# Kernel tuning notes

Measured on AMD Instinct MI355X. Metric: run time of the kernel, lower is better.

Reference implementation:

```python
import jax, jax.numpy as jnp
import numpy as np

N_BONDS = 16777216
N_ATOMS = 1048576
N_TYPES = 16


def setup_inputs() -> dict:
    key = jax.random.key(0)
    k1, k2, k3, k4, k5, k6 = jax.random.split(key, 6)
    # bond orders kept strictly positive so BO**p_be2 and its grad are finite
    bo_sigma = jax.random.uniform(k1, (N_BONDS,), jnp.float32, 0.05, 1.0)
    bo_pi = jax.random.uniform(k2, (N_BONDS,), jnp.float32, 0.05, 1.0)
    bo_pipi = jax.random.uniform(k3, (N_BONDS,), jnp.float32, 0.05, 1.0)
    bond_type = jax.random.randint(k4, (N_BONDS,), 0, N_TYPES, jnp.int32)
    atom_i = jax.random.randint(k5, (N_BONDS,), 0, N_ATOMS, jnp.int32)
    # columns: De_sigma, De_pi, De_pipi, p_be1, p_be2 (positive, O(1))
    bond_params = jax.random.uniform(k6, (N_TYPES, 5), jnp.float32, 0.1, 1.0)
    return {
        "bond_type": bond_type,
        "atom_i": atom_i,
        "bo_sigma": bo_sigma,
        "bo_pi": bo_pi,
        "bo_pipi": bo_pipi,
        "bond_params": bond_params,
        "n_atoms": N_ATOMS,
    }


def reference(bond_type, atom_i, bo_sigma, bo_pi, bo_pipi, bond_params, n_atoms):
    # Gather per-bond-type parameters: [E, 5]
    p = bond_params[bond_type]
    de_s, de_p, de_pp, p_be1, p_be2 = (p[:, 0], p[:, 1], p[:, 2], p[:, 3], p[:, 4])
    # ReaxFF bond energy per bond
    e_bond = (-de_s * bo_sigma * jnp.exp(p_be1 * (1.0 - bo_sigma ** p_be2))
              - de_p * bo_pi
              - de_pp * bo_pipi)
    # Scatter-reduce to per-atom energy
    e_atom = jax.ops.segment_sum(e_bond, atom_i, num_segments=n_atoms)
    return e_atom
```

## Files before the change

kernel.cpp:

```cpp
#include <hip/hip_runtime.h>


typedef float f32x4 __attribute__((ext_vector_type(4)));
typedef int   i32x4 __attribute__((ext_vector_type(4)));
typedef unsigned u32;

#define NB     512
#define RANGE  2048
#define SHIFT  11
#define CB     8192
#define TB     256
#define PADQ   8u

__device__ __forceinline__ u32 f32_to_bf16_bits(float f) {
    u32 u = __float_as_uint(f);
    return ((u + 0x7FFFu + ((u >> 16) & 1u)) >> 16) & 0xFFFFu;
}

__global__ __launch_bounds__(TB) void count_kernel(
        const i32x4* __restrict__ atom_i, u32* __restrict__ counts,
        int round_start) {
    __shared__ u32 hist[4][NB];
    int tid = threadIdx.x, w = tid >> 6;
    for (int i = tid; i < 4 * NB; i += TB) ((u32*)hist)[i] = 0u;
    __syncthreads();
    long base4 = ((long)round_start + (long)blockIdx.x * CB) >> 2;
#pragma unroll
    for (int it = 0; it < CB / (TB * 4); ++it) {
        i32x4 a = __builtin_nontemporal_load(&atom_i[base4 + it * TB + tid]);
        atomicAdd(&hist[w][(u32)a.x >> SHIFT], 1u);
        atomicAdd(&hist[w][(u32)a.y >> SHIFT], 1u);
        atomicAdd(&hist[w][(u32)a.z >> SHIFT], 1u);
        atomicAdd(&hist[w][(u32)a.w >> SHIFT], 1u);
    }
    __syncthreads();
    for (int b = tid; b < NB; b += TB)
        counts[(size_t)blockIdx.x * NB + b] =
            hist[0][b] + hist[1][b] + hist[2][b] + hist[3][b];
}

__global__ __launch_bounds__(TB) void scan_cols_kernel(
        const u32* __restrict__ counts, u32* __restrict__ offs,
        u32* __restrict__ total, int nsb) {
    __shared__ u32 sc[TB];
    int b = blockIdx.x, t = threadIdx.x;
    int vpt = nsb >> 8;
    u32 v[16];
    u32 s = 0;
    for (int k = 0; k < vpt; ++k) {
        u32 c = counts[(size_t)(t * vpt + k) * NB + b];
        c = (c + PADQ - 1u) & ~(PADQ - 1u);
        v[k] = s; s += c;
    }
    sc[t] = s;
    __syncthreads();
    for (int off = 1; off < TB; off <<= 1) {
        u32 u = (t >= off) ? sc[t - off] : 0u;
        __syncthreads();
        sc[t] += u;
        __syncthreads();
    }
    u32 excl = sc[t] - s;
    for (int k = 0; k < vpt; ++k)
        offs[(size_t)(t * vpt + k) * NB + b] = excl + v[k];
    if (t == TB - 1) total[b] = sc[t];
}

__global__ __launch_bounds__(TB, 4) void partition_kernel(
        const i32x4* __restrict__ bt, const i32x4* __restrict__ ai,
        const f32x4* __restrict__ bs_, const f32x4* __restrict__ bp_,
        const f32x4* __restrict__ bpp_, const float* __restrict__ bond_params,
        const u32* __restrict__ counts, const u32* __restrict__ offs,
        const u32* __restrict__ total, u32* __restrict__ arena,
        int round_start) {
    __shared__ u32   sorted[CB];
    __shared__ u32   cnt[NB], cur[NB], gstart[NB];
    __shared__ u32   scanb[TB];
    __shared__ float4 sp_a[16];
    __shared__ float  sp_b[16];

    int tid = threadIdx.x, sb = blockIdx.x;
    if (tid < 16) {
        const float* p = bond_params + tid * 5;
        sp_a[tid] = make_float4(p[0], p[1], p[2], p[3]);
        sp_b[tid] = p[4];
    }
    u32 c0 = counts[(size_t)sb * NB + 2 * tid];
    u32 c1 = counts[(size_t)sb * NB + 2 * tid + 1];
    cnt[2 * tid] = c0; cnt[2 * tid + 1] = c1;
    scanb[tid] = c0 + c1;
    __syncthreads();
    for (int off = 1; off < TB; off <<= 1) {
        u32 u = (tid >= off) ? scanb[tid - off] : 0u;
        __syncthreads();
        scanb[tid] += u;
        __syncthreads();
    }
    u32 excl = scanb[tid] - (c0 + c1);
    cur[2 * tid] = excl; cur[2 * tid + 1] = excl + c0;
    __syncthreads();
    u32 t0 = total[2 * tid], t1 = total[2 * tid + 1];
    scanb[tid] = t0 + t1;
    __syncthreads();
    for (int off = 1; off < TB; off <<= 1) {
        u32 u = (tid >= off) ? scanb[tid - off] : 0u;
        __syncthreads();
        scanb[tid] += u;
        __syncthreads();
    }
    u32 excl2 = scanb[tid] - (t0 + t1);
    gstart[2 * tid]     = excl2 + offs[(size_t)sb * NB + 2 * tid];
    gstart[2 * tid + 1] = excl2 + t0 + offs[(size_t)sb * NB + 2 * tid + 1];
    __syncthreads();

    long base4 = ((long)round_start + (long)sb * CB) >> 2;
#pragma unroll
    for (int it = 0; it < CB / (TB * 4); ++it) {
        long idx = base4 + it * TB + tid;
        i32x4 t  = __builtin_nontemporal_load(&bt[idx]);
        i32x4 a  = __builtin_nontemporal_load(&ai[idx]);
        f32x4 s  = __builtin_nontemporal_load(&bs_[idx]);
        f32x4 p  = __builtin_nontemporal_load(&bp_[idx]);
        f32x4 pp = __builtin_nontemporal_load(&bpp_[idx]);
#pragma unroll
        for (int k = 0; k < 4; ++k) {
            u32 ak = (u32)a[k];
            float4 pa = sp_a[t[k]];
            float  pb = sp_b[t[k]];
            float pw = __powf(s[k], pb);
            float e  = -pa.x * s[k] * __expf(pa.w * (1.0f - pw))
                       - pa.y * p[k] - pa.z * pp[k];
            u32 b = ak >> SHIFT;
            u32 pos = atomicAdd(&cur[b], 1u);
            sorted[pos] = ((ak & (RANGE - 1u)) << 16) | f32_to_bf16_bits(e);
        }
    }
    __syncthreads();

    int w = tid >> 6, lane = tid & 63;
    int gi = lane >> 4, j0 = lane & 15;
    for (int b = w * 4 + gi; b < NB; b += 16) {
        u32 end = cur[b], len = cnt[b], ls = end - len;
        u32 plen = (len + PADQ - 1u) & ~(PADQ - 1u);
        u32 g = gstart[b];
        for (u32 j = j0; j < plen; j += 16u)
            arena[g + j] = (j < len) ? sorted[ls + j] : 0u;
    }
}

__global__ __launch_bounds__(TB, 4) void accum_kernel(
        const u32* __restrict__ arena, const u32* __restrict__ total,
        float* __restrict__ out, int add_prev) {
    __shared__ float acc[4][RANGE];
    __shared__ u32 red[TB];
    int tid = threadIdx.x, w = tid >> 6, b = blockIdx.x;
    u32 part = 0;
    for (int i = tid; i < b; i += TB) part += total[i];
    red[tid] = part;
    for (int i = tid; i < RANGE; i += TB) {
        acc[0][i] = 0.f; acc[1][i] = 0.f; acc[2][i] = 0.f; acc[3][i] = 0.f;
    }
    __syncthreads();
    for (int s = TB / 2; s > 0; s >>= 1) {
        if (tid < s) red[tid] += red[tid + s];
        __syncthreads();
    }
    u32 s0 = red[0];
    u32 n  = total[b];
    const uint4* src = (const uint4*)(arena + s0);
    for (u32 j = tid; j < (n >> 2); j += TB) {
        uint4 e = src[j];
        if (e.x) atomicAdd(&acc[w][e.x >> 16], __uint_as_float((e.x & 0xFFFFu) << 16));
        if (e.y) atomicAdd(&acc[w][e.y >> 16], __uint_as_float((e.y & 0xFFFFu) << 16));
        if (e.z) atomicAdd(&acc[w][e.z >> 16], __uint_as_float((e.z & 0xFFFFu) << 16));
        if (e.w) atomicAdd(&acc[w][e.w >> 16], __uint_as_float((e.w & 0xFFFFu) << 16));
    }
    __syncthreads();
    size_t ob = (size_t)b * RANGE;
    for (int i = tid; i < RANGE; i += TB) {
        float v = acc[0][i] + acc[1][i] + acc[2][i] + acc[3][i];
        if (add_prev) v += out[ob + i];
        out[ob + i] = v;
    }
}

__global__ __launch_bounds__(TB) void zero_kernel(f32x4* __restrict__ p, int n4) {
    int i = blockIdx.x * blockDim.x + threadIdx.x;
    if (i < n4) p[i] = (f32x4)(0.f);
}

__global__ __launch_bounds__(TB) void atomic_fallback_kernel(
        const i32x4* __restrict__ bt, const i32x4* __restrict__ ai,
        const f32x4* __restrict__ bs_, const f32x4* __restrict__ bp_,
        const f32x4* __restrict__ bpp_, const float* __restrict__ bond_params,
        float* __restrict__ out, int n4) {
    __shared__ float sp[80];
    if (threadIdx.x < 80) sp[threadIdx.x] = bond_params[threadIdx.x];
    __syncthreads();
    int i = blockIdx.x * blockDim.x + threadIdx.x;
    if (i >= n4) return;
    i32x4 t  = bt[i]; i32x4 a = ai[i];
    f32x4 s  = bs_[i]; f32x4 p = bp_[i]; f32x4 pp = bpp_[i];
#pragma unroll
    for (int k = 0; k < 4; ++k) {
        const float* pr = sp + t[k] * 5;
        float pw = __powf(s[k], pr[4]);
        float e  = -pr[0] * s[k] * __expf(pr[3] * (1.0f - pw))
                   - pr[1] * p[k] - pr[2] * pp[k];
        unsafeAtomicAdd(&out[a[k]], e);
    }
}

extern "C" void kernel_launch(void* const* d_in, const int* in_sizes, int n_in,
                              void* d_out, int out_size, void* d_ws, size_t ws_size,
                              hipStream_t stream) {
    const int*   bond_type   = (const int*)  d_in[0];
    const int*   atom_i      = (const int*)  d_in[1];
    const float* bo_sigma    = (const float*)d_in[2];
    const float* bo_pi       = (const float*)d_in[3];
    const float* bo_pipi     = (const float*)d_in[4];
    const float* bond_params = (const float*)d_in[5];
    float*       e_atom      = (float*)d_out;

    const int n_bonds = in_sizes[0];
    const int n_atoms = out_size;

    int NR = 0;
    if (n_atoms == (NB << SHIFT)) {
        const int cands[5] = {1, 2, 4, 8, 16};
        for (int ci = 0; ci < 5; ++ci) {
            int r = cands[ci];
            if (n_bonds % (r * CB)) continue;
            int cpr = n_bonds / r, nsb = cpr / CB;
            if (nsb % 256 || nsb < 256 || nsb > 4096) continue;
            size_t arena_worst = (size_t)cpr + (size_t)(PADQ - 1) * NB * nsb;
            size_t need = arena_worst * 4 + 2 * (size_t)nsb * NB * 4 + (size_t)NB * 4;
            if (need <= ws_size) { NR = r; break; }
        }
    }

    if (NR) {
        const int cpr = n_bonds / NR, nsb = cpr / CB;
        size_t arena_worst = (size_t)cpr + (size_t)(PADQ - 1) * NB * nsb;
        u32* arena  = (u32*)d_ws;
        u32* counts = arena + arena_worst;
        u32* offs   = counts + (size_t)nsb * NB;
        u32* total  = offs + (size_t)nsb * NB;
        for (int r = 0; r < NR; ++r) {
            int rs = r * cpr;
            count_kernel<<<nsb, TB, 0, stream>>>((const i32x4*)atom_i, counts, rs);
            scan_cols_kernel<<<NB, TB, 0, stream>>>(counts, offs, total, nsb);
            partition_kernel<<<nsb, TB, 0, stream>>>(
                (const i32x4*)bond_type, (const i32x4*)atom_i,
                (const f32x4*)bo_sigma, (const f32x4*)bo_pi, (const f32x4*)bo_pipi,
                bond_params, counts, offs, total, arena, rs);
            accum_kernel<<<NB, TB, 0, stream>>>(arena, total, e_atom, r ? 1 : 0);
        }
    } else {
        int zn4 = n_atoms / 4;
        zero_kernel<<<(zn4 + TB - 1) / TB, TB, 0, stream>>>((f32x4*)e_atom, zn4);
        int n4 = n_bonds / 4;
        atomic_fallback_kernel<<<(n4 + TB - 1) / TB, TB, 0, stream>>>(
            (const i32x4*)bond_type, (const i32x4*)atom_i,
            (const f32x4*)bo_sigma, (const f32x4*)bo_pi, (const f32x4*)bo_pipi,
            bond_params, e_atom, n4);
    }
}
```

Baseline: 439.3 us.

## Shrink partition chunk, hoist bucket base scan, use 16-bit counts and wave scans

Adds a 4096-bond chunk option for the count and partition kernels and prefers it, so each partition block uses half the LDS and more blocks fit per CU (launch bound raised to 7). The per-block scan of bucket totals moves into a separate single-block base_kernel that writes gbase, which accum also reads instead of re-reducing totals. Per-block counts are stored as u16 and the LDS Hillis-Steele scans become wave-shuffle scans. The cost is an extra tiny launch per round, twice as many chunks with more padded slots in the arena, and more count/offs traffic in the column scan.

New measurement: 457.5 us. +4.2%, slower.

```diff
diff --git a/kernel.cpp b/kernel.cpp
--- a/kernel.cpp
+++ b/kernel.cpp
@@ -4,11 +4,11 @@
 typedef float f32x4 __attribute__((ext_vector_type(4)));
 typedef int   i32x4 __attribute__((ext_vector_type(4)));
 typedef unsigned u32;
+typedef unsigned short u16;
 
 #define NB     512
 #define RANGE  2048
 #define SHIFT  11
-#define CB     8192
 #define TB     256
 #define PADQ   8u
 
@@ -17,16 +17,33 @@
     return ((u + 0x7FFFu + ((u >> 16) & 1u)) >> 16) & 0xFFFFu;
 }
 
+__device__ __forceinline__ u32 block_excl_scan(u32 v, u32* wsum, int tid) {
+    u32 s = v;
+#pragma unroll
+    for (int off = 1; off < 64; off <<= 1) {
+        u32 n = __shfl_up(s, off);
+        if ((tid & 63) >= off) s += n;
+    }
+    if ((tid & 63) == 63) wsum[tid >> 6] = s;
+    __syncthreads();
+    int w = tid >> 6;
+    u32 wb = 0;
+#pragma unroll
+    for (int ww = 0; ww < 3; ++ww) wb += (ww < w) ? wsum[ww] : 0u;
+    return wb + s - v;
+}
+
+template<int CBK>
 __global__ __launch_bounds__(TB) void count_kernel(
-        const i32x4* __restrict__ atom_i, u32* __restrict__ counts,
+        const i32x4* __restrict__ atom_i, u16* __restrict__ counts,
         int round_start) {
     __shared__ u32 hist[4][NB];
     int tid = threadIdx.x, w = tid >> 6;
     for (int i = tid; i < 4 * NB; i += TB) ((u32*)hist)[i] = 0u;
     __syncthreads();
-    long base4 = ((long)round_start + (long)blockIdx.x * CB) >> 2;
-#pragma unroll
-    for (int it = 0; it < CB / (TB * 4); ++it) {
+    long base4 = ((long)round_start + (long)blockIdx.x * CBK) >> 2;
+#pragma unroll
+    for (int it = 0; it < CBK / (TB * 4); ++it) {
         i32x4 a = __builtin_nontemporal_load(&atom_i[base4 + it * TB + tid]);
         atomicAdd(&hist[w][(u32)a.x >> SHIFT], 1u);
         atomicAdd(&hist[w][(u32)a.y >> SHIFT], 1u);
@@ -36,11 +53,11 @@
     __syncthreads();
     for (int b = tid; b < NB; b += TB)
         counts[(size_t)blockIdx.x * NB + b] =
-            hist[0][b] + hist[1][b] + hist[2][b] + hist[3][b];
+            (u16)(hist[0][b] + hist[1][b] + hist[2][b] + hist[3][b]);
 }
 
 __global__ __launch_bounds__(TB) void scan_cols_kernel(
-        const u32* __restrict__ counts, u32* __restrict__ offs,
+        const u16* __restrict__ counts, u32* __restrict__ offs,
         u32* __restrict__ total, int nsb) {
     __shared__ u32 sc[TB];
     int b = blockIdx.x, t = threadIdx.x;
@@ -66,16 +83,27 @@
     if (t == TB - 1) total[b] = sc[t];
 }
 
-__global__ __launch_bounds__(TB, 4) void partition_kernel(
+__global__ __launch_bounds__(TB) void base_kernel(
+        const u32* __restrict__ total, u32* __restrict__ gbase) {
+    __shared__ u32 wsum[4];
+    int t = threadIdx.x;
+    u32 t0 = total[2 * t], t1 = total[2 * t + 1];
+    u32 excl = block_excl_scan(t0 + t1, wsum, t);
+    gbase[2 * t]     = excl;
+    gbase[2 * t + 1] = excl + t0;
+}
+
+template<int CBK, int MINB>
+__global__ __launch_bounds__(TB, MINB) void partition_kernel(
         const i32x4* __restrict__ bt, const i32x4* __restrict__ ai,
         const f32x4* __restrict__ bs_, const f32x4* __restrict__ bp_,
         const f32x4* __restrict__ bpp_, const float* __restrict__ bond_params,
-        const u32* __restrict__ counts, const u32* __restrict__ offs,
-        const u32* __restrict__ total, u32* __restrict__ arena,
+        const u16* __restrict__ counts, const u32* __restrict__ offs,
+        const u32* __restrict__ gbase, u32* __restrict__ arena,
         int round_start) {
-    __shared__ u32   sorted[CB];
-    __shared__ u32   cnt[NB], cur[NB], gstart[NB];
-    __shared__ u32   scanb[TB];
+    __shared__ u32   sorted[CBK];
+    __shared__ u32   start_[NB], cur[NB];
+    __shared__ u32   wsum[4];
     __shared__ float4 sp_a[16];
     __shared__ float  sp_b[16];
 
@@ -85,37 +113,16 @@
         sp_a[tid] = make_float4(p[0], p[1], p[2], p[3]);
         sp_b[tid] = p[4];
     }
-    u32 c0 = counts[(size_t)sb * NB + 2 * tid];
-    u32 c1 = counts[(size_t)sb * NB + 2 * tid + 1];
-    cnt[2 * tid] = c0; cnt[2 * tid + 1] = c1;
-    scanb[tid] = c0 + c1;
-    __syncthreads();
-    for (int off = 1; off < TB; off <<= 1) {
-        u32 u = (tid >= off) ? scanb[tid - off] : 0u;
-        __syncthreads();
-        scanb[tid] += u;
-        __syncthreads();
-    }
-    u32 excl = scanb[tid] - (c0 + c1);
-    cur[2 * tid] = excl; cur[2 * tid + 1] = excl + c0;
-    __syncthreads();
-    u32 t0 = total[2 * tid], t1 = total[2 * tid + 1];
-    scanb[tid] = t0 + t1;
-    __syncthreads();
-    for (int off = 1; off < TB; off <<= 1) {
-        u32 u = (tid >= off) ? scanb[tid - off] : 0u;
-        __syncthreads();
-        scanb[tid] += u;
-        __syncthreads();
-    }
-    u32 excl2 = scanb[tid] - (t0 + t1);
-    gstart[2 * tid]     = excl2 + offs[(size_t)sb * NB + 2 * tid];
-    gstart[2 * tid + 1] = excl2 + t0 + offs[(size_t)sb * NB + 2 * tid + 1];
-    __syncthreads();
-
-    long base4 = ((long)round_start + (long)sb * CB) >> 2;
-#pragma unroll
-    for (int it = 0; it < CB / (TB * 4); ++it) {
+    u32 c01 = ((const u32*)(counts + (size_t)sb * NB))[tid];
+    u32 c0 = c01 & 0xFFFFu, c1 = c01 >> 16;
+    u32 excl = block_excl_scan(c0 + c1, wsum, tid);
+    start_[2 * tid]     = excl;       cur[2 * tid]     = excl;
+    start_[2 * tid + 1] = excl + c0;  cur[2 * tid + 1] = excl + c0;
+    __syncthreads();
+
+    long base4 = ((long)round_start + (long)sb * CBK) >> 2;
+#pragma unroll
+    for (int it = 0; it < CBK / (TB * 4); ++it) {
         long idx = base4 + it * TB + tid;
         i32x4 t  = __builtin_nontemporal_load(&bt[idx]);
         i32x4 a  = __builtin_nontemporal_load(&ai[idx]);
@@ -137,35 +144,29 @@
     }
     __syncthreads();
 
+    constexpr int LG  = (CBK >= 8192) ? 16 : 8;
+    constexpr int GPW = 64 / LG;
     int w = tid >> 6, lane = tid & 63;
-    int gi = lane >> 4, j0 = lane & 15;
-    for (int b = w * 4 + gi; b < NB; b += 16) {
-        u32 end = cur[b], len = cnt[b], ls = end - len;
+    int gi = lane / LG, j0 = lane % LG;
+    for (int b = w * GPW + gi; b < NB; b += 4 * GPW) {
+        u32 end = cur[b], ls = start_[b], len = end - ls;
         u32 plen = (len + PADQ - 1u) & ~(PADQ - 1u);
-        u32 g = gstart[b];
-        for (u32 j = j0; j < plen; j += 16u)
+        u32 g = gbase[b] + offs[(size_t)sb * NB + b];
+        for (u32 j = j0; j < plen; j += LG)
             arena[g + j] = (j < len) ? sorted[ls + j] : 0u;
     }
 }
 
 __global__ __launch_bounds__(TB, 4) void accum_kernel(
         const u32* __restrict__ arena, const u32* __restrict__ total,
-        float* __restrict__ out, int add_prev) {
+        const u32* __restrict__ gbase, float* __restrict__ out, int add_prev) {
     __shared__ float acc[4][RANGE];
-    __shared__ u32 red[TB];
     int tid = threadIdx.x, w = tid >> 6, b = blockIdx.x;
-    u32 part = 0;
-    for (int i = tid; i < b; i += TB) part += total[i];
-    red[tid] = part;
     for (int i = tid; i < RANGE; i += TB) {
         acc[0][i] = 0.f; acc[1][i] = 0.f; acc[2][i] = 0.f; acc[3][i] = 0.f;
     }
     __syncthreads();
-    for (int s = TB / 2; s > 0; s >>= 1) {
-        if (tid < s) red[tid] += red[tid + s];
-        __syncthreads();
-    }
-    u32 s0 = red[0];
+    u32 s0 = gbase[b];
     u32 n  = total[b];
     const uint4* src = (const uint4*)(arena + s0);
     for (u32 j = tid; j < (n >> 2); j += TB) {
@@ -225,36 +226,59 @@
     const int n_bonds = in_sizes[0];
     const int n_atoms = out_size;
 
-    int NR = 0;
+    int cfg_cb = 0, cfg_nr = 0;
     if (n_atoms == (NB << SHIFT)) {
-        const int cands[5] = {1, 2, 4, 8, 16};
-        for (int ci = 0; ci < 5; ++ci) {
-            int r = cands[ci];
-            if (n_bonds % (r * CB)) continue;
-            int cpr = n_bonds / r, nsb = cpr / CB;
+        const int prefs[10][2] = {
+            {4096, 1}, {4096, 2}, {8192, 1}, {8192, 2}, {4096, 4},
+            {8192, 4}, {4096, 8}, {8192, 8}, {4096, 16}, {8192, 16}};
+        for (int ci = 0; ci < 10 && !cfg_nr; ++ci) {
+            int cb = prefs[ci][0], r = prefs[ci][1];
+            if (n_bonds % (r * cb)) continue;
+            long cpr = (long)n_bonds / r, nsb = cpr / cb;
             if (nsb % 256 || nsb < 256 || nsb > 4096) continue;
             size_t arena_worst = (size_t)cpr + (size_t)(PADQ - 1) * NB * nsb;
-            size_t need = arena_worst * 4 + 2 * (size_t)nsb * NB * 4 + (size_t)NB * 4;
-            if (need <= ws_size) { NR = r; break; }
+            size_t need = arena_worst * 4
+                        + (size_t)nsb * NB * 4
+                        + (size_t)NB * 4
+                        + (size_t)NB * 4
+                        + (size_t)nsb * NB * 2
+                        + 256;
+            if (need <= ws_size) { cfg_cb = cb; cfg_nr = r; }
         }
     }
 
-    if (NR) {
-        const int cpr = n_bonds / NR, nsb = cpr / CB;
+    if (cfg_nr) {
+        const int NR = cfg_nr, cpr = n_bonds / NR, nsb = cpr / cfg_cb;
         size_t arena_worst = (size_t)cpr + (size_t)(PADQ - 1) * NB * nsb;
         u32* arena  = (u32*)d_ws;
-        u32* counts = arena + arena_worst;
-        u32* offs   = counts + (size_t)nsb * NB;
+        u32* offs   = arena + arena_worst;
         u32* total  = offs + (size_t)nsb * NB;
+        u32* gbase  = total + NB;
+        u16* counts = (u16*)(gbase + NB);
         for (int r = 0; r < NR; ++r) {
             int rs = r * cpr;
-            count_kernel<<<nsb, TB, 0, stream>>>((const i32x4*)atom_i, counts, rs);
+            if (cfg_cb == 4096)
+                count_kernel<4096><<<nsb, TB, 0, stream>>>(
+                    (const i32x4*)atom_i, counts, rs);
+            else
+                count_kernel<8192><<<nsb, TB, 0, stream>>>(
+                    (const i32x4*)atom_i, counts, rs);
             scan_cols_kernel<<<NB, TB, 0, stream>>>(counts, offs, total, nsb);
-            partition_kernel<<<nsb, TB, 0, stream>>>(
-                (const i32x4*)bond_type, (const i32x4*)atom_i,
-                (const f32x4*)bo_sigma, (const f32x4*)bo_pi, (const f32x4*)bo_pipi,
-                bond_params, counts, offs, total, arena, rs);
-            accum_kernel<<<NB, TB, 0, stream>>>(arena, total, e_atom, r ? 1 : 0);
+            base_kernel<<<1, TB, 0, stream>>>(total, gbase);
+            if (cfg_cb == 4096)
+                partition_kernel<4096, 7><<<nsb, TB, 0, stream>>>(
+                    (const i32x4*)bond_type, (const i32x4*)atom_i,
+                    (const f32x4*)bo_sigma, (const f32x4*)bo_pi,
+                    (const f32x4*)bo_pipi, bond_params,
+                    counts, offs, gbase, arena, rs);
+            else
+                partition_kernel<8192, 4><<<nsb, TB, 0, stream>>>(
+                    (const i32x4*)bond_type, (const i32x4*)atom_i,
+                    (const f32x4*)bo_sigma, (const f32x4*)bo_pi,
+                    (const f32x4*)bo_pipi, bond_params,
+                    counts, offs, gbase, arena, rs);
+            accum_kernel<<<NB, TB, 0, stream>>>(arena, total, gbase, e_atom,
+                                                r ? 1 : 0);
         }
     } else {
         int zn4 = n_atoms / 4;
```

## Use 64 coarse atom buckets with split accumulation and partial merge

Applied to the files above, without the earlier changes.

Atoms are now partitioned into 64 wide buckets of 16384 atoms instead of 512 buckets of 2048. That shrinks the per-block histogram and prefix-scan work, lets counts be stored as u16, and makes each bucket's writes into the arena longer and more contiguous. A tiny base kernel does the global bucket scan once, replacing the per-block redundant scans. Accumulation runs with 4 splits per bucket in 1024-thread blocks, each holding a 64KB LDS accumulator; the partial sums go to global memory and a merge kernel adds them. The trade-off is lower LDS occupancy and extra global traffic for the partials, plus one more launch.

Measured after the change: 423.6 us. 3.6% less time.

```diff
diff --git a/kernel.cpp b/kernel.cpp
--- a/kernel.cpp
+++ b/kernel.cpp
@@ -1,16 +1,19 @@
 #include <hip/hip_runtime.h>
 
 
-typedef float f32x4 __attribute__((ext_vector_type(4)));
-typedef int   i32x4 __attribute__((ext_vector_type(4)));
+typedef float    f32x4 __attribute__((ext_vector_type(4)));
+typedef int      i32x4 __attribute__((ext_vector_type(4)));
+typedef unsigned u32x4 __attribute__((ext_vector_type(4)));
 typedef unsigned u32;
-
-#define NB     512
-#define RANGE  2048
-#define SHIFT  11
+typedef unsigned short u16;
+
+#define NBUK   64
+#define RANGEK 16384
+#define SHIFTK 14
 #define CB     8192
 #define TB     256
-#define PADQ   8u
+#define PADQ   16u
+#define SPLITS 4
 
 __device__ __forceinline__ u32 f32_to_bf16_bits(float f) {
     u32 u = __float_as_uint(f);
@@ -18,37 +21,37 @@
 }
 
 __global__ __launch_bounds__(TB) void count_kernel(
-        const i32x4* __restrict__ atom_i, u32* __restrict__ counts,
+        const i32x4* __restrict__ atom_i, u16* __restrict__ counts,
         int round_start) {
-    __shared__ u32 hist[4][NB];
+    __shared__ u32 hist[4][NBUK];
     int tid = threadIdx.x, w = tid >> 6;
-    for (int i = tid; i < 4 * NB; i += TB) ((u32*)hist)[i] = 0u;
+    if (tid < 4 * NBUK) ((u32*)hist)[tid] = 0u;
     __syncthreads();
     long base4 = ((long)round_start + (long)blockIdx.x * CB) >> 2;
 #pragma unroll
     for (int it = 0; it < CB / (TB * 4); ++it) {
         i32x4 a = __builtin_nontemporal_load(&atom_i[base4 + it * TB + tid]);
-        atomicAdd(&hist[w][(u32)a.x >> SHIFT], 1u);
-        atomicAdd(&hist[w][(u32)a.y >> SHIFT], 1u);
-        atomicAdd(&hist[w][(u32)a.z >> SHIFT], 1u);
-        atomicAdd(&hist[w][(u32)a.w >> SHIFT], 1u);
-    }
-    __syncthreads();
-    for (int b = tid; b < NB; b += TB)
-        counts[(size_t)blockIdx.x * NB + b] =
-            hist[0][b] + hist[1][b] + hist[2][b] + hist[3][b];
+        atomicAdd(&hist[w][(u32)a.x >> SHIFTK], 1u);
+        atomicAdd(&hist[w][(u32)a.y >> SHIFTK], 1u);
+        atomicAdd(&hist[w][(u32)a.z >> SHIFTK], 1u);
+        atomicAdd(&hist[w][(u32)a.w >> SHIFTK], 1u);
+    }
+    __syncthreads();
+    if (tid < NBUK)
+        counts[(size_t)blockIdx.x * NBUK + tid] =
+            (u16)(hist[0][tid] + hist[1][tid] + hist[2][tid] + hist[3][tid]);
 }
 
 __global__ __launch_bounds__(TB) void scan_cols_kernel(
-        const u32* __restrict__ counts, u32* __restrict__ offs,
+        const u16* __restrict__ counts, u32* __restrict__ offs,
         u32* __restrict__ total, int nsb) {
     __shared__ u32 sc[TB];
     int b = blockIdx.x, t = threadIdx.x;
     int vpt = nsb >> 8;
-    u32 v[16];
+    u32 v[8];
     u32 s = 0;
     for (int k = 0; k < vpt; ++k) {
-        u32 c = counts[(size_t)(t * vpt + k) * NB + b];
+        u32 c = counts[(size_t)(t * vpt + k) * NBUK + b];
         c = (c + PADQ - 1u) & ~(PADQ - 1u);
         v[k] = s; s += c;
     }
@@ -62,20 +65,32 @@
     }
     u32 excl = sc[t] - s;
     for (int k = 0; k < vpt; ++k)
-        offs[(size_t)(t * vpt + k) * NB + b] = excl + v[k];
+        offs[(size_t)(t * vpt + k) * NBUK + b] = excl + v[k];
     if (t == TB - 1) total[b] = sc[t];
+}
+
+__global__ __launch_bounds__(64) void base_kernel(
+        const u32* __restrict__ total, u32* __restrict__ gbase) {
+    int t = threadIdx.x;
+    u32 v = total[t];
+    u32 s = v;
+#pragma unroll
+    for (int off = 1; off < 64; off <<= 1) {
+        u32 n = __shfl_up(s, off);
+        if (t >= off) s += n;
+    }
+    gbase[t] = s - v;
 }
 
 __global__ __launch_bounds__(TB, 4) void partition_kernel(
         const i32x4* __restrict__ bt, const i32x4* __restrict__ ai,
         const f32x4* __restrict__ bs_, const f32x4* __restrict__ bp_,
         const f32x4* __restrict__ bpp_, const float* __restrict__ bond_params,
-        const u32* __restrict__ counts, const u32* __restrict__ offs,
-        const u32* __restrict__ total, u32* __restrict__ arena,
+        const u16* __restrict__ counts, const u32* __restrict__ offs,
+        const u32* __restrict__ gbase, u32* __restrict__ arena,
         int round_start) {
     __shared__ u32   sorted[CB];
-    __shared__ u32   cnt[NB], cur[NB], gstart[NB];
-    __shared__ u32   scanb[TB];
+    __shared__ u32   start_[NBUK], cur[NBUK], gofs[NBUK];
     __shared__ float4 sp_a[16];
     __shared__ float  sp_b[16];
 
@@ -85,32 +100,19 @@
         sp_a[tid] = make_float4(p[0], p[1], p[2], p[3]);
         sp_b[tid] = p[4];
     }
-    u32 c0 = counts[(size_t)sb * NB + 2 * tid];
-    u32 c1 = counts[(size_t)sb * NB + 2 * tid + 1];
-    cnt[2 * tid] = c0; cnt[2 * tid + 1] = c1;
-    scanb[tid] = c0 + c1;
-    __syncthreads();
-    for (int off = 1; off < TB; off <<= 1) {
-        u32 u = (tid >= off) ? scanb[tid - off] : 0u;
-        __syncthreads();
-        scanb[tid] += u;
-        __syncthreads();
-    }
-    u32 excl = scanb[tid] - (c0 + c1);
-    cur[2 * tid] = excl; cur[2 * tid + 1] = excl + c0;
-    __syncthreads();
-    u32 t0 = total[2 * tid], t1 = total[2 * tid + 1];
-    scanb[tid] = t0 + t1;
-    __syncthreads();
-    for (int off = 1; off < TB; off <<= 1) {
-        u32 u = (tid >= off) ? scanb[tid - off] : 0u;
-        __syncthreads();
-        scanb[tid] += u;
-        __syncthreads();
-    }
-    u32 excl2 = scanb[tid] - (t0 + t1);
-    gstart[2 * tid]     = excl2 + offs[(size_t)sb * NB + 2 * tid];
-    gstart[2 * tid + 1] = excl2 + t0 + offs[(size_t)sb * NB + 2 * tid + 1];
+    if (tid < 64) {
+        u32 c = counts[(size_t)sb * NBUK + tid];
+        u32 s = c;
+#pragma unroll
+        for (int off = 1; off < 64; off <<= 1) {
+            u32 n = __shfl_up(s, off);
+            if (tid >= off) s += n;
+        }
+        u32 excl = s - c;
+        start_[tid] = excl;
+        cur[tid]    = excl;
+        gofs[tid]   = gbase[tid] + offs[(size_t)sb * NBUK + tid];
+    }
     __syncthreads();
 
     long base4 = ((long)round_start + (long)sb * CB) >> 2;
@@ -130,58 +132,64 @@
             float pw = __powf(s[k], pb);
             float e  = -pa.x * s[k] * __expf(pa.w * (1.0f - pw))
                        - pa.y * p[k] - pa.z * pp[k];
-            u32 b = ak >> SHIFT;
+            u32 b = ak >> SHIFTK;
             u32 pos = atomicAdd(&cur[b], 1u);
-            sorted[pos] = ((ak & (RANGE - 1u)) << 16) | f32_to_bf16_bits(e);
+            sorted[pos] = ((ak & (RANGEK - 1u)) << 16) | f32_to_bf16_bits(e);
         }
     }
     __syncthreads();
 
     int w = tid >> 6, lane = tid & 63;
-    int gi = lane >> 4, j0 = lane & 15;
-    for (int b = w * 4 + gi; b < NB; b += 16) {
-        u32 end = cur[b], len = cnt[b], ls = end - len;
+    for (int b = w; b < NBUK; b += 4) {
+        u32 end = cur[b], ls = start_[b], len = end - ls;
         u32 plen = (len + PADQ - 1u) & ~(PADQ - 1u);
-        u32 g = gstart[b];
-        for (u32 j = j0; j < plen; j += 16u)
+        u32 g = gofs[b];
+        for (u32 j = lane; j < plen; j += 64u)
             arena[g + j] = (j < len) ? sorted[ls + j] : 0u;
     }
 }
 
-__global__ __launch_bounds__(TB, 4) void accum_kernel(
+__global__ __launch_bounds__(1024) void accum_kernel(
         const u32* __restrict__ arena, const u32* __restrict__ total,
-        float* __restrict__ out, int add_prev) {
-    __shared__ float acc[4][RANGE];
-    __shared__ u32 red[TB];
-    int tid = threadIdx.x, w = tid >> 6, b = blockIdx.x;
-    u32 part = 0;
-    for (int i = tid; i < b; i += TB) part += total[i];
-    red[tid] = part;
-    for (int i = tid; i < RANGE; i += TB) {
-        acc[0][i] = 0.f; acc[1][i] = 0.f; acc[2][i] = 0.f; acc[3][i] = 0.f;
-    }
-    __syncthreads();
-    for (int s = TB / 2; s > 0; s >>= 1) {
-        if (tid < s) red[tid] += red[tid + s];
-        __syncthreads();
-    }
-    u32 s0 = red[0];
+        const u32* __restrict__ gbase, float* __restrict__ partials) {
+    __shared__ float acc[RANGEK];
+    int tid = threadIdx.x;
+    int b = blockIdx.x >> 2, sp = blockIdx.x & 3;
+    f32x4* a4 = (f32x4*)acc;
+#pragma unroll
+    for (int i = 0; i < RANGEK / 4 / 1024; ++i)
+        a4[i * 1024 + tid] = (f32x4)(0.f);
+    __syncthreads();
+    u32 s0 = gbase[b];
     u32 n  = total[b];
-    const uint4* src = (const uint4*)(arena + s0);
-    for (u32 j = tid; j < (n >> 2); j += TB) {
-        uint4 e = src[j];
-        if (e.x) atomicAdd(&acc[w][e.x >> 16], __uint_as_float((e.x & 0xFFFFu) << 16));
-        if (e.y) atomicAdd(&acc[w][e.y >> 16], __uint_as_float((e.y & 0xFFFFu) << 16));
-        if (e.z) atomicAdd(&acc[w][e.z >> 16], __uint_as_float((e.z & 0xFFFFu) << 16));
-        if (e.w) atomicAdd(&acc[w][e.w >> 16], __uint_as_float((e.w & 0xFFFFu) << 16));
-    }
-    __syncthreads();
-    size_t ob = (size_t)b * RANGE;
-    for (int i = tid; i < RANGE; i += TB) {
-        float v = acc[0][i] + acc[1][i] + acc[2][i] + acc[3][i];
-        if (add_prev) v += out[ob + i];
-        out[ob + i] = v;
-    }
+    u32 qs = n >> 4;
+    const u32x4* src = (const u32x4*)(arena + s0) + (size_t)sp * qs;
+    for (u32 j = tid; j < qs; j += 1024) {
+        u32x4 e = __builtin_nontemporal_load(&src[j]);
+        atomicAdd(&acc[e.x >> 16], __uint_as_float((e.x & 0xFFFFu) << 16));
+        atomicAdd(&acc[e.y >> 16], __uint_as_float((e.y & 0xFFFFu) << 16));
+        atomicAdd(&acc[e.z >> 16], __uint_as_float((e.z & 0xFFFFu) << 16));
+        atomicAdd(&acc[e.w >> 16], __uint_as_float((e.w & 0xFFFFu) << 16));
+    }
+    __syncthreads();
+    f32x4* pr = (f32x4*)(partials + ((size_t)sp * NBUK + b) * RANGEK);
+#pragma unroll
+    for (int i = 0; i < RANGEK / 4 / 1024; ++i)
+        pr[i * 1024 + tid] = a4[i * 1024 + tid];
+}
+
+__global__ __launch_bounds__(TB) void merge_kernel(
+        const float* __restrict__ partials, float* __restrict__ out,
+        int n_atoms, int add_prev) {
+    int i = blockIdx.x * TB + threadIdx.x;
+    const f32x4* p0 = (const f32x4*)partials;
+    const f32x4* p1 = (const f32x4*)(partials + (size_t)n_atoms);
+    const f32x4* p2 = (const f32x4*)(partials + 2 * (size_t)n_atoms);
+    const f32x4* p3 = (const f32x4*)(partials + 3 * (size_t)n_atoms);
+    f32x4* o4 = (f32x4*)out;
+    f32x4 v = p0[i] + p1[i] + p2[i] + p3[i];
+    if (add_prev) v += o4[i];
+    o4[i] = v;
 }
 
 __global__ __launch_bounds__(TB) void zero_kernel(f32x4* __restrict__ p, int n4) {
@@ -225,36 +233,47 @@
     const int n_bonds = in_sizes[0];
     const int n_atoms = out_size;
 
-    int NR = 0;
-    if (n_atoms == (NB << SHIFT)) {
+    int cfg_nr = 0;
+    if (n_atoms == (NBUK << SHIFTK)) {
         const int cands[5] = {1, 2, 4, 8, 16};
-        for (int ci = 0; ci < 5; ++ci) {
+        for (int ci = 0; ci < 5 && !cfg_nr; ++ci) {
             int r = cands[ci];
             if (n_bonds % (r * CB)) continue;
-            int cpr = n_bonds / r, nsb = cpr / CB;
+            long cpr = (long)n_bonds / r, nsb = cpr / CB;
             if (nsb % 256 || nsb < 256 || nsb > 4096) continue;
-            size_t arena_worst = (size_t)cpr + (size_t)(PADQ - 1) * NB * nsb;
-            size_t need = arena_worst * 4 + 2 * (size_t)nsb * NB * 4 + (size_t)NB * 4;
-            if (need <= ws_size) { NR = r; break; }
-        }
-    }
-
-    if (NR) {
-        const int cpr = n_bonds / NR, nsb = cpr / CB;
-        size_t arena_worst = (size_t)cpr + (size_t)(PADQ - 1) * NB * nsb;
-        u32* arena  = (u32*)d_ws;
-        u32* counts = arena + arena_worst;
-        u32* offs   = counts + (size_t)nsb * NB;
-        u32* total  = offs + (size_t)nsb * NB;
+            size_t arena_worst = (size_t)cpr + (size_t)(PADQ - 1) * NBUK * nsb;
+            size_t need = arena_worst * 4
+                        + (size_t)nsb * NBUK * 4
+                        + (size_t)NBUK * 8
+                        + (size_t)nsb * NBUK * 2
+                        + (size_t)SPLITS * n_atoms * 4
+                        + 256;
+            if (need <= ws_size) cfg_nr = r;
+        }
+    }
+
+    if (cfg_nr) {
+        const int NR = cfg_nr, cpr = n_bonds / NR, nsb = cpr / CB;
+        size_t arena_worst = (size_t)cpr + (size_t)(PADQ - 1) * NBUK * nsb;
+        u32*   arena    = (u32*)d_ws;
+        u32*   offs     = arena + arena_worst;
+        u32*   total    = offs + (size_t)nsb * NBUK;
+        u32*   gbase    = total + NBUK;
+        u16*   counts   = (u16*)(gbase + NBUK);
+        float* partials = (float*)(counts + (size_t)nsb * NBUK);
         for (int r = 0; r < NR; ++r) {
             int rs = r * cpr;
             count_kernel<<<nsb, TB, 0, stream>>>((const i32x4*)atom_i, counts, rs);
-            scan_cols_kernel<<<NB, TB, 0, stream>>>(counts, offs, total, nsb);
+            scan_cols_kernel<<<NBUK, TB, 0, stream>>>(counts, offs, total, nsb);
+            base_kernel<<<1, 64, 0, stream>>>(total, gbase);
             partition_kernel<<<nsb, TB, 0, stream>>>(
                 (const i32x4*)bond_type, (const i32x4*)atom_i,
                 (const f32x4*)bo_sigma, (const f32x4*)bo_pi, (const f32x4*)bo_pipi,
-                bond_params, counts, offs, total, arena, rs);
-            accum_kernel<<<NB, TB, 0, stream>>>(arena, total, e_atom, r ? 1 : 0);
+                bond_params, counts, offs, gbase, arena, rs);
+            accum_kernel<<<NBUK * SPLITS, 1024, 0, stream>>>(
+                arena, total, gbase, partials);
+            merge_kernel<<<n_atoms / 4 / TB, TB, 0, stream>>>(
+                partials, e_atom, n_atoms, r ? 1 : 0);
         }
     } else {
         int zn4 = n_atoms / 4;
```
